# Kernel tuning notes

Hardware: AMD Instinct MI355X
Metric: run time of the kernel (lower is better)

## Reference

```python
import jax, jax.numpy as jnp
import numpy as np
import math

B, T, H, W, C = 2, 8, 32, 32, 512
DEPTH = 2
HEADS = 16
GH = 8            # global FAVOR+ heads (first GH heads, as in performer-pytorch)
DH = C // HEADS   # 32
WIN = C // 8      # 64 = local window size
FF = 2 * C
NB_F = int(DH * math.log(DH))  # 110 random features (performer default)


def _ortho_proj(m, d, rng):
    # gaussian orthogonal random matrix, scaling=0 (row norms ~ chi(d))
    blocks = []
    for _ in range(m // d + 1):
        q, _ = np.linalg.qr(rng.standard_normal((d, d)))
        blocks.append(q.T)
    Q = np.concatenate(blocks, 0)[:m]
    mult = np.linalg.norm(rng.standard_normal((m, d)), axis=1)
    return (mult[:, None] * Q).astype(np.float32)


def setup_inputs():
    rng = np.random.default_rng(0)
    g = lambda *s: jnp.asarray(rng.standard_normal(s) * 0.02, jnp.float32)
    z = lambda *s: jnp.zeros(s, jnp.float32)
    o = lambda *s: jnp.ones(s, jnp.float32)
    p = {}
    p["x"] = jnp.asarray(rng.standard_normal((B, T, H, W, C)), jnp.float32)
    p["ln1_g"], p["ln1_b"] = o(DEPTH, C), z(DEPTH, C)
    p["Wq"], p["bq"] = g(DEPTH, C, C), z(DEPTH, C)
    p["Wk"], p["bk"] = g(DEPTH, C, C), z(DEPTH, C)
    p["Wv"], p["bv"] = g(DEPTH, C, C), z(DEPTH, C)
    p["Wo"], p["bo"] = g(DEPTH, C, C), z(DEPTH, C)
    p["proj"] = jnp.asarray(np.stack([_ortho_proj(NB_F, DH, rng) for _ in range(DEPTH)]))
    p["ln2_g"], p["ln2_b"] = o(DEPTH, C), z(DEPTH, C)
    p["W1"], p["b1"] = g(DEPTH, C, FF), z(DEPTH, FF)
    p["W2"], p["b2"] = g(DEPTH, FF, C), z(DEPTH, C)
    return p


def _ln(x, g, b):
    m = x.mean(-1, keepdims=True)
    v = x.var(-1, keepdims=True)
    return (x - m) / jnp.sqrt(v + 1e-5) * g + b


def _softmax_kernel(x, proj, is_query):
    # FAVOR+ positive softmax features. x: [b,h,n,d], proj: [m,d]
    d = x.shape[-1]
    m = proj.shape[0]
    dn = d ** -0.25
    dd = jnp.einsum('bhnd,md->bhnm', x * dn, proj)
    diag = jnp.sum(x * x, -1, keepdims=True) * 0.5 * (dn * dn)
    if is_query:
        stab = jnp.max(dd, axis=-1, keepdims=True)
    else:
        stab = jnp.max(dd, axis=(-1, -2), keepdims=True)
    return (m ** -0.5) * (jnp.exp(dd - diag - stab) + 1e-4)


def _rot_half(x):
    x1, x2 = jnp.split(x, 2, axis=-1)
    return jnp.concatenate([-x2, x1], axis=-1)


def _local_attn(q, k, v, win=WIN):
    # non-causal sliding window, look_backward=1, look_forward=1
    b, hh, n, d = q.shape
    nw = n // win
    qb = q.reshape(b, hh, nw, win, d)
    kb = k.reshape(b, hh, nw, win, d)
    vb = v.reshape(b, hh, nw, win, d)

    def look(t):
        p = jnp.pad(t, ((0, 0), (0, 0), (1, 1), (0, 0), (0, 0)))
        return jnp.concatenate([p[:, :, :-2], p[:, :, 1:-1], p[:, :, 2:]], 3)

    kk, vv = look(kb), look(vb)
    posb = jnp.arange(n).reshape(nw, win)
    pp = jnp.pad(posb, ((1, 1), (0, 0)), constant_values=-1)
    kpos = jnp.concatenate([pp[:-2], pp[1:-1], pp[2:]], 1)
    mask = (kpos == -1)[None, None, :, None, :]
    s = jnp.einsum('bhwid,bhwjd->bhwij', qb * (d ** -0.5), kk)
    s = jnp.where(mask, -1e9, s)
    a = jax.nn.softmax(s, axis=-1)
    o = jnp.einsum('bhwij,bhwjd->bhwid', a, vv)
    return o.reshape(b, hh, n, d)


def _forward(x, ln1_g, ln1_b, Wq, bq, Wk, bk, Wv, bv, Wo, bo, proj, ln2_g, ln2_b, W1, b1, W2, b2):
    Bx, Tx, Hx, Wx, Cx = x.shape
    n = Tx * Hx * Wx
    h = x.reshape(Bx, n, Cx)
    # rotary rel-pos for local heads (local-attention rel_pos_emb_config)
    inv_freq = 1.0 / (10000.0 ** (jnp.arange(0, DH, 2, dtype=jnp.float32) / DH))
    freqs = jnp.arange(n, dtype=jnp.float32)[:, None] * inv_freq[None, :]
    emb = jnp.concatenate([freqs, freqs], -1)
    sin, cos = jnp.sin(emb), jnp.cos(emb)

    for l in range(DEPTH):
        y = _ln(h, ln1_g[l], ln1_b[l])
        q = (y @ Wq[l] + bq[l]).reshape(Bx, n, HEADS, DH).transpose(0, 2, 1, 3)
        k = (y @ Wk[l] + bk[l]).reshape(Bx, n, HEADS, DH).transpose(0, 2, 1, 3)
        v = (y @ Wv[l] + bv[l]).reshape(Bx, n, HEADS, DH).transpose(0, 2, 1, 3)
        gq, lq = q[:, :GH], q[:, GH:]
        gk, lk = k[:, :GH], k[:, GH:]
        gv, lv = v[:, :GH], v[:, GH:]
        # global: FAVOR+ linear attention
        qp = _softmax_kernel(gq, proj[l], True)
        kp = _softmax_kernel(gk, proj[l], False)
        Dinv = 1.0 / jnp.einsum('bhnm,bhm->bhn', qp, kp.sum(-2))
        ctx = jnp.einsum('bhnm,bhnd->bhmd', kp, gv)
        og = jnp.einsum('bhmd,bhnm,bhn->bhnd', ctx, qp, Dinv)
        # local: windowed attention with rotary pos emb
        lqr = lq * cos + _rot_half(lq) * sin
        lkr = lk * cos + _rot_half(lk) * sin
        ol = _local_attn(lqr, lkr, lv)
        o = jnp.concatenate([og, ol], 1).transpose(0, 2, 1, 3).reshape(Bx, n, Cx)
        h = h + o @ Wo[l] + bo[l]
        y = _ln(h, ln2_g[l], ln2_b[l])
        h = h + jax.nn.gelu(y @ W1[l] + b1[l], approximate=False) @ W2[l] + b2[l]
    return h.reshape(Bx, Tx, Hx, Wx, Cx)


def reference(x, ln1_g, ln1_b, Wq, bq, Wk, bk, Wv, bv, Wo, bo, proj, ln2_g, ln2_b, W1, b1, W2, b2):
    return _forward(x, ln1_g, ln1_b, Wq, bq, Wk, bk, Wv, bv, Wo, bo, proj, ln2_g, ln2_b, W1, b1, W2, b2)
```

## Files before the change

kernel.cpp:

```cpp
#include <hip/hip_runtime.h>
#include <math.h>

namespace {

constexpr int BATCH = 2;
constexpr int NTOK  = 8192;
constexpr int MROWS = 16384;
constexpr int C     = 512;
constexpr int GH    = 8;
constexpr int DH    = 32;
constexpr int WIN   = 64;
constexpr int NW    = 128;
constexpr int FF    = 1024;
constexpr int NBF   = 110;
constexpr int NBFP  = 128;

constexpr float F_DN     = 0.42044820762685725f;
constexpr float F_RNORM  = 0.09534625892455924f;
constexpr float F_LSCALE = 0.17677669529663687f;

typedef __attribute__((ext_vector_type(8))) short bf16x8;
typedef __attribute__((ext_vector_type(4))) float f32x4;

__device__ __forceinline__ ushort f2b(float f){
  unsigned u = __float_as_uint(f);
  unsigned r = u + 0x7FFFu + ((u >> 16) & 1u);
  return (ushort)(r >> 16);
}
__device__ __forceinline__ float b2f(ushort u){
  return __uint_as_float((unsigned)u << 16);
}

__device__ __forceinline__ void gload16(const void* g, void* l){
  __builtin_amdgcn_global_load_lds((const __attribute__((address_space(1))) void*)g,
                                   (__attribute__((address_space(3))) void*)l, 16, 0, 0);
}

__global__ void k_tables(float* __restrict__ cost, float* __restrict__ sint){
  int idx = blockIdx.x*256 + threadIdx.x;
  if (idx >= NTOK*16) return;
  int pos = idx >> 4, f = idx & 15;
  float inv = powf(10000.f, -(float)f/16.f);
  float ang = (float)pos * inv;
  cost[idx] = cosf(ang);
  sint[idx] = sinf(ang);
}

__global__ __launch_bounds__(256) void k_wcvt_all(const float* __restrict__ Wq, const float* __restrict__ Wk,
     const float* __restrict__ Wv, const float* __restrict__ Wo, const float* __restrict__ W1,
     const float* __restrict__ W2, ushort* __restrict__ wt){
  __shared__ float t[32][33];
  int id = blockIdx.x;
  int l = id >> 11;
  int r = id & 2047;
  const float* src; ushort* dst; int K, N, bx, by;
  if (r < 1024){
    int mat = r >> 8, tt = r & 255;
    bx = tt & 15; by = tt >> 4; K = 512; N = 512;
    src = ((mat == 0) ? Wq : (mat == 1) ? Wk : (mat == 2) ? Wv : Wo) + (size_t)l*262144;
    dst = wt + (size_t)l*2097152 + (size_t)mat*262144;
  } else if (r < 1536){
    int tt = r - 1024;
    bx = tt & 31; by = tt >> 5; K = 512; N = 1024;
    src = W1 + (size_t)l*524288;
    dst = wt + (size_t)l*2097152 + 1048576;
  } else {
    int tt = r - 1536;
    bx = tt & 15; by = tt >> 4; K = 1024; N = 512;
    src = W2 + (size_t)l*524288;
    dst = wt + (size_t)l*2097152 + 1572864;
  }
  int tx = threadIdx.x & 31, ty = threadIdx.x >> 5;
  #pragma unroll
  for (int rr = ty; rr < 32; rr += 8) t[rr][tx] = src[(size_t)(by*32+rr)*N + bx*32 + tx];
  __syncthreads();
  #pragma unroll
  for (int rr = ty; rr < 32; rr += 8) dst[(size_t)(bx*32+rr)*K + by*32 + tx] = f2b(t[tx][rr]);
}

__global__ __launch_bounds__(256) void k_ln(const float* __restrict__ x, const float* __restrict__ g,
                     const float* __restrict__ b, ushort* __restrict__ y){
  int row = blockIdx.x, t = threadIdx.x;
  const float* xr = x + (size_t)row*C;
  float2 v = *(const float2*)(xr + 2*t);
  float s = v.x + v.y, ss = v.x*v.x + v.y*v.y;
  #pragma unroll
  for (int o = 32; o; o >>= 1){ s += __shfl_down(s, o); ss += __shfl_down(ss, o); }
  __shared__ float rs[4], rss[4];
  int wv = t >> 6, ln = t & 63;
  if (ln == 0){ rs[wv] = s; rss[wv] = ss; }
  __syncthreads();
  float S = rs[0]+rs[1]+rs[2]+rs[3], SS = rss[0]+rss[1]+rss[2]+rss[3];
  float mean = S * (1.f/C);
  float var  = SS * (1.f/C) - mean*mean;
  float rstd = rsqrtf(var + 1e-5f);
  float2 gg = *(const float2*)(g + 2*t);
  float2 bb = *(const float2*)(b + 2*t);
  ushort2 ov;
  ov.x = f2b((v.x - mean)*rstd*gg.x + bb.x);
  ov.y = f2b((v.y - mean)*rstd*gg.y + bb.y);
  *(ushort2*)(y + (size_t)row*C + 2*t) = ov;
}

template<int ACT, int OBF, int QKV>
__global__ __launch_bounds__(256) void k_mgemm(const ushort* __restrict__ A, const ushort* __restrict__ Bt,
      const float* __restrict__ bias, const float* __restrict__ bias2, const float* __restrict__ bias3,
      const float* __restrict__ res, float* __restrict__ outf, ushort* __restrict__ outb,
      const float* __restrict__ cosT, const float* __restrict__ sinT, int Nd, int Kd){
  __shared__ ushort As[2][128*32];
  __shared__ ushort Bs[2][128*32];
  int tid = threadIdx.x;
  int lane = tid & 63, wave = tid >> 6;
  int wr = wave >> 1, wc = wave & 1;
  int gx = gridDim.x;
  int nwg = gx * (int)gridDim.y;
  int bid = (int)(blockIdx.y*gx + blockIdx.x);
  int swz = (bid & 7)*(nwg >> 3) + (bid >> 3);
  int row0 = (swz / gx)*128, col0 = (swz % gx)*128;
  f32x4 acc[4][4] = {};
  int nt = Kd >> 5;

  #define STAGE(buf, kt) {                                                        \
    int k0_ = (kt)*32;                                                            \
    _Pragma("unroll")                                                             \
    for (int cc = 0; cc < 2; cc++){                                               \
      int off = (wave*2 + cc)*1024 + lane*16;                                     \
      int r_ = off >> 6, ke_ = (off & 63) >> 1;                                   \
      gload16(A  + (size_t)(row0 + r_)*Kd + k0_ + ke_,                            \
              (char*)As[buf] + (wave*2 + cc)*1024);                               \
      gload16(Bt + (size_t)(col0 + r_)*Kd + k0_ + ke_,                            \
              (char*)Bs[buf] + (wave*2 + cc)*1024);                               \
    }                                                                             \
  }

  STAGE(0, 0);
  __syncthreads();

  for (int t = 0; t < nt; t++){
    int cur = t & 1;
    bf16x8 af[4], bfr[4];
    #pragma unroll
    for (int m = 0; m < 4; m++)
      af[m] = *(const bf16x8*)((const char*)As[cur] + (wr*64 + m*16 + (lane&15))*64 + (lane>>4)*16);
    #pragma unroll
    for (int n = 0; n < 4; n++)
      bfr[n] = *(const bf16x8*)((const char*)Bs[cur] + (wc*64 + n*16 + (lane&15))*64 + (lane>>4)*16);
    if (t + 1 < nt) STAGE(cur^1, t+1);
    __builtin_amdgcn_s_setprio(1);
    #pragma unroll
    for (int m = 0; m < 4; m++)
      #pragma unroll
      for (int n = 0; n < 4; n++)
        acc[m][n] = __builtin_amdgcn_mfma_f32_16x16x32_bf16(af[m], bfr[n], acc[m][n], 0, 0, 0);
    __builtin_amdgcn_s_setprio(0);
    __syncthreads();
  }
  #undef STAGE

  if (QKV){
    #pragma unroll
    for (int m = 0; m < 4; m++){
      int rbase = row0 + wr*64 + m*16 + (lane>>4)*4;
      #pragma unroll
      for (int np = 0; np < 2; np++){
        int n0 = 2*np, n1 = n0 + 1;
        int ccol = col0 + wc*64 + n0*16 + (lane&15);
        int bid2 = ccol >> 9;
        int cl  = ccol & 511;
        const float* bp = (bid2 == 0) ? bias : (bid2 == 1) ? bias2 : bias3;
        float b0 = bp[cl], b1 = bp[cl+16];
        bool dorope = (bid2 < 2) && (cl >= 256);
        ushort* obase = outb + (size_t)bid2*MROWS*C;
        int d = lane & 15;
        #pragma unroll
        for (int r = 0; r < 4; r++){
          int grow = rbase + r;
          float a  = acc[m][n0][r] + b0;
          float bb = acc[m][n1][r] + b1;
          if (dorope){
            int pos = grow & (NTOK-1);
            float cv = cosT[pos*16 + d], sv = sinT[pos*16 + d];
            float na = a*cv - bb*sv;
            float nb = bb*cv + a*sv;
            a = na; bb = nb;
          }
          obase[(size_t)grow*C + cl]      = f2b(a);
          obase[(size_t)grow*C + cl + 16] = f2b(bb);
        }
      }
    }
    return;
  }
  #pragma unroll
  for (int m = 0; m < 4; m++){
    int rbase = row0 + wr*64 + m*16 + (lane>>4)*4;
    #pragma unroll
    for (int n = 0; n < 4; n++){
      int ccol = col0 + wc*64 + n*16 + (lane&15);
      float bv = bias[ccol];
      #pragma unroll
      for (int r = 0; r < 4; r++){
        int grow = rbase + r;
        float vv = acc[m][n][r] + bv;
        if (ACT == 1) vv = 0.5f*vv*(1.f + erff(vv*0.7071067811865476f));
        if (res) vv += res[(size_t)grow*Nd + ccol];
        if (OBF) outb[(size_t)grow*Nd + ccol] = f2b(vv);
        else     outf[(size_t)grow*Nd + ccol] = vv;
      }
    }
  }
}

__global__ __launch_bounds__(256) void k_ctx3(const ushort* __restrict__ k, const ushort* __restrict__ v,
        const float* __restrict__ proj, float* __restrict__ ctxp, float* __restrict__ ksump){
  int bh = blockIdx.x >> 5, chunk = blockIdx.x & 31;
  int b = bh >> 3, h = bh & 7;
  __shared__ __align__(16) ushort pl[NBFP*40];
  __shared__ __align__(16) ushort Ps[NBFP*72];
  __shared__ __align__(16) ushort Vt[48*72];
  __shared__ float dgl[256];
  int tid = threadIdx.x;
  int lane = tid & 63, wave = tid >> 6;
  int c = lane & 15, g = lane >> 4;
  int i0 = chunk*256;

  for (int idx = tid; idx < NBFP*32; idx += 256){
    int f = idx >> 5, d = idx & 31;
    pl[f*40 + d] = (f < NBF) ? f2b(proj[f*32 + d]*F_DN) : (ushort)0;
  }
  const ushort* kbase = k + ((size_t)b*NTOK + i0)*C + h*DH;
  const ushort* vbase = v + ((size_t)b*NTOK + i0)*C + h*DH;
  #pragma unroll
  for (int s = 0; s < 4; s++){
    bf16x8 kf = *(const bf16x8*)(kbase + (size_t)(s*64 + wave*16 + c)*C + g*8);
    const ushort* kp_ = (const ushort*)&kf;
    float sq = 0.f;
    #pragma unroll
    for (int j = 0; j < 8; j++){ float vv = b2f(kp_[j]); sq += vv*vv; }
    sq += __shfl_xor(sq, 16);
    sq += __shfl_xor(sq, 32);
    if (g == 0) dgl[s*64 + wave*16 + c] = 0.5f*F_DN*F_DN*sq;
  }
  for (int idx = tid; idx < 15*72; idx += 256) Vt[33*72 + idx] = 0;

  f32x4 zz = {0.f, 0.f, 0.f, 0.f};
  f32x4 acc[2][3] = {};

  for (int s = 0; s < 4; s++){
    __syncthreads();
    {
      int r = tid >> 2, part = tid & 3;
      uint4 vv = *(const uint4*)(vbase + (size_t)(s*64 + r)*C + part*8);
      const ushort* vp = (const ushort*)&vv;
      #pragma unroll
      for (int j = 0; j < 8; j++) Vt[(part*8+j)*72 + r] = vp[j];
      if (tid < 64) Vt[32*72 + tid] = 0x3F80;
    }
    bf16x8 af = *(const bf16x8*)(kbase + (size_t)(s*64 + wave*16 + c)*C + g*8);
    #pragma unroll
    for (int ft = 0; ft < 8; ft++){
      bf16x8 bf = *(const bf16x8*)(pl + (ft*16 + c)*40 + g*8);
      f32x4 dd = __builtin_amdgcn_mfma_f32_16x16x32_bf16(af, bf, zz, 0, 0, 0);
      int feat = ft*16 + c;
      bool fvalid = feat < NBF;
      ushort pb[4];
      #pragma unroll
      for (int r = 0; r < 4; r++){
        float kp = 0.f;
        if (fvalid){
          float dg_ = dgl[s*64 + wave*16 + g*4 + r];
          kp = F_RNORM*(__expf(dd[r] - dg_) + 1e-4f);
        }
        pb[r] = f2b(kp);
      }
      uint2 pd;
      pd.x = (unsigned)pb[0] | ((unsigned)pb[1] << 16);
      pd.y = (unsigned)pb[2] | ((unsigned)pb[3] << 16);
      *(uint2*)(Ps + (ft*16 + c)*72 + wave*16 + g*4) = pd;
    }
    __syncthreads();
    #pragma unroll
    for (int i = 0; i < 2; i++){
      int ft = wave*2 + i;
      #pragma unroll
      for (int kk = 0; kk < 2; kk++){
        bf16x8 ap = *(const bf16x8*)(Ps + (ft*16 + c)*72 + kk*32 + g*8);
        #pragma unroll
        for (int nt = 0; nt < 3; nt++){
          bf16x8 bv = *(const bf16x8*)(Vt + (nt*16 + c)*72 + kk*32 + g*8);
          acc[i][nt] = __builtin_amdgcn_mfma_f32_16x16x32_bf16(ap, bv, acc[i][nt], 0, 0, 0);
        }
      }
    }
  }
  size_t pbase = (size_t)(bh*32 + chunk)*NBF;
  #pragma unroll
  for (int i = 0; i < 2; i++){
    int ftb = (wave*2 + i)*16;
    #pragma unroll
    for (int r = 0; r < 4; r++){
      int feat = ftb + g*4 + r;
      if (feat < NBF){
        #pragma unroll
        for (int nt = 0; nt < 2; nt++)
          ctxp[(pbase + feat)*DH + nt*16 + c] = acc[i][nt][r];
        if (c == 0) ksump[pbase + feat] = acc[i][2][r];
      }
    }
  }
}

__global__ void k_ctxred(const float* __restrict__ ctxp, const float* __restrict__ ksump,
                         float* __restrict__ ctx, float* __restrict__ ksum){
  int bh = blockIdx.x / NBF, m = blockIdx.x % NBF;
  int t = threadIdx.x;
  if (t < DH){
    float s = 0.f;
    for (int c = 0; c < 32; c++) s += ctxp[((size_t)(bh*32 + c)*NBF + m)*DH + t];
    ctx[((size_t)bh*NBF + m)*DH + t] = s;
  } else if (t == DH){
    float s = 0.f;
    for (int c = 0; c < 32; c++) s += ksump[(size_t)(bh*32 + c)*NBF + m];
    ksum[bh*NBF + m] = s;
  }
}

__global__ __launch_bounds__(256) void k_qattn3(const ushort* __restrict__ q, const float* __restrict__ proj,
        const float* __restrict__ ctx, const float* __restrict__ ksum, ushort* __restrict__ o){
  int bh = blockIdx.x >> 7, chunk = blockIdx.x & 127;
  int b = bh >> 3, h = bh & 7;
  __shared__ __align__(16) ushort pl[NBFP*40];
  __shared__ __align__(16) ushort ql[64*40];
  __shared__ __align__(16) ushort ctl[32*136];
  __shared__ __align__(16) ushort Ps[64*136];
  __shared__ float ksl[NBFP];
  __shared__ float dgl[64];
  __shared__ float dvl[64];
  int tid = threadIdx.x;
  int lane = tid & 63, wave = tid >> 6;
  int c = lane & 15, g = lane >> 4;
  int i0 = chunk*64;

  for (int idx = tid; idx < NBFP*32; idx += 256){
    int f = idx >> 5, d = idx & 31;
    pl[f*40 + d] = (f < NBF) ? f2b(proj[f*32 + d]*F_DN) : (ushort)0;
  }
  {
    int row = tid >> 2, part = tid & 3;
    uint4 qq = *(const uint4*)(q + (size_t)(b*NTOK + i0 + row)*C + h*DH + part*8);
    *(uint4*)(ql + row*40 + part*8) = qq;
    const ushort* qp_ = (const ushort*)&qq;
    float sq = 0.f;
    #pragma unroll
    for (int j = 0; j < 8; j++){ float vv = b2f(qp_[j]); sq += vv*vv; }
    sq += __shfl_xor(sq, 1);
    sq += __shfl_xor(sq, 2);
    if (part == 0) dgl[row] = 0.5f*F_DN*F_DN*sq;
  }
  for (int idx = tid; idx < 32*NBFP; idx += 256){
    int d = idx >> 7, f = idx & 127;
    float vv = (f < NBF) ? ctx[((size_t)bh*NBF + f)*DH + d] : 0.f;
    ctl[d*136 + f] = f2b(vv);
  }
  if (tid < NBFP) ksl[tid] = (tid < NBF) ? ksum[bh*NBF + tid] : 0.f;
  __syncthreads();

  f32x4 zz = {0.f, 0.f, 0.f, 0.f};
  bf16x8 qf = *(const bf16x8*)(ql + (wave*16 + c)*40 + g*8);
  f32x4 st[8];
  #pragma unroll
  for (int mt = 0; mt < 8; mt++){
    bf16x8 af = *(const bf16x8*)(pl + (mt*16 + c)*40 + g*8);
    st[mt] = __builtin_amdgcn_mfma_f32_16x16x32_bf16(af, qf, zz, 0, 0, 0);
  }
  float mx = -1e30f;
  #pragma unroll
  for (int mt = 0; mt < 8; mt++)
    #pragma unroll
    for (int r = 0; r < 4; r++){
      int feat = mt*16 + g*4 + r;
      if (feat < NBF) mx = fmaxf(mx, st[mt][r]);
    }
  mx = fmaxf(mx, __shfl_xor(mx, 16));
  mx = fmaxf(mx, __shfl_xor(mx, 32));
  float diagv = dgl[wave*16 + c];
  float dv = 0.f;
  #pragma unroll
  for (int mt = 0; mt < 8; mt++){
    ushort pb[4];
    #pragma unroll
    for (int r = 0; r < 4; r++){
      int feat = mt*16 + g*4 + r;
      float qp = 0.f;
      if (feat < NBF) qp = F_RNORM*(__expf(st[mt][r] - diagv - mx) + 1e-4f);
      ushort qb = f2b(qp);
      pb[r] = qb;
      dv += b2f(qb)*ksl[feat];
    }
    uint2 pd;
    pd.x = (unsigned)pb[0] | ((unsigned)pb[1] << 16);
    pd.y = (unsigned)pb[2] | ((unsigned)pb[3] << 16);
    *(uint2*)(Ps + (wave*16 + c)*136 + mt*16 + g*4) = pd;
  }
  dv += __shfl_xor(dv, 16);
  dv += __shfl_xor(dv, 32);
  if (g == 0) dvl[wave*16 + c] = 1.f/dv;
  __syncthreads();

  #pragma unroll
  for (int n = 0; n < 2; n++){
    f32x4 acc = zz;
    #pragma unroll
    for (int kk = 0; kk < 4; kk++){
      bf16x8 ap = *(const bf16x8*)(Ps  + (wave*16 + c)*136 + kk*32 + g*8);
      bf16x8 bc = *(const bf16x8*)(ctl + (n*16 + c)*136    + kk*32 + g*8);
      acc = __builtin_amdgcn_mfma_f32_16x16x32_bf16(ap, bc, acc, 0, 0, 0);
    }
    #pragma unroll
    for (int r = 0; r < 4; r++){
      int qrow = wave*16 + g*4 + r;
      float val = acc[r]*dvl[qrow];
      o[(size_t)(b*NTOK + i0 + qrow)*C + h*DH + n*16 + c] = f2b(val);
    }
  }
}

__global__ __launch_bounds__(256) void k_local2(const ushort* __restrict__ q, const ushort* __restrict__ k,
        const ushort* __restrict__ v, ushort* __restrict__ o){
  int blk = blockIdx.x;
  int w = blk & (NW-1);
  int rem = blk >> 7;
  int hl = rem & 7, b = rem >> 3;
  int hd = GH + hl;
  __shared__ __align__(16) ushort Ks[192*32];
  __shared__ __align__(16) ushort Vt[32*200];
  __shared__ __align__(16) ushort Ps[4*16*200];
  int tid = threadIdx.x;
  int lane = tid & 63, wave = tid >> 6;
  int c = lane & 15, g = lane >> 4;

  const ushort* kbase = k + (size_t)b*NTOK*C + hd*DH;
  const ushort* vbase = v + (size_t)b*NTOK*C + hd*DH;
  #pragma unroll
  for (int s = 0; s < 3; s++){
    int ch = tid + s*256;
    int row = ch >> 2, part = ch & 3;
    int kp = min(max((w-1)*WIN + row, 0), NTOK-1);
    gload16(kbase + (size_t)kp*C + part*8, (char*)Ks + (s*256 + wave*64)*16);
  }
  #pragma unroll
  for (int s = 0; s < 3; s++){
    int ch = tid + s*256;
    int row = ch >> 2, part = ch & 3;
    int kp = min(max((w-1)*WIN + row, 0), NTOK-1);
    uint4 vv = *(const uint4*)(vbase + (size_t)kp*C + part*8);
    const ushort* vp = (const ushort*)&vv;
    #pragma unroll
    for (int j = 0; j < 8; j++) Vt[(part*8+j)*200 + row] = vp[j];
  }
  int qrow = w*WIN + wave*16 + c;
  bf16x8 qf = *(const bf16x8*)(q + ((size_t)b*NTOK + qrow)*C + hd*DH + g*8);
  asm volatile("s_waitcnt vmcnt(0)" ::: "memory");
  __syncthreads();

  f32x4 zz = {0.f, 0.f, 0.f, 0.f};
  f32x4 st[12];
  #pragma unroll
  for (int t = 0; t < 12; t++){
    bf16x8 af = *(const bf16x8*)(Ks + (16*t + c)*32 + g*8);
    st[t] = __builtin_amdgcn_mfma_f32_16x16x32_bf16(af, qf, zz, 0, 0, 0);
  }
  int t0 = (w == 0) ? 4 : 0;
  int t1 = (w == NW-1) ? 8 : 12;
  float lsum = 0.f;
  ushort* pw = Ps + wave*3200 + c*200;
  #pragma unroll
  for (int t = 0; t < 12; t++){
    bool valid = (t >= t0) && (t < t1);
    float p0 = valid ? __expf(st[t][0]*F_LSCALE) : 0.f;
    float p1 = valid ? __expf(st[t][1]*F_LSCALE) : 0.f;
    float p2 = valid ? __expf(st[t][2]*F_LSCALE) : 0.f;
    float p3 = valid ? __expf(st[t][3]*F_LSCALE) : 0.f;
    lsum += (p0+p1)+(p2+p3);
    uint2 pd;
    pd.x = (unsigned)f2b(p0) | ((unsigned)f2b(p1) << 16);
    pd.y = (unsigned)f2b(p2) | ((unsigned)f2b(p3) << 16);
    *(uint2*)(pw + 16*t + 4*g) = pd;
  }
  lsum += __shfl_xor(lsum, 16);
  lsum += __shfl_xor(lsum, 32);

  f32x4 oc0 = zz, oc1 = zz;
  #pragma unroll
  for (int kb = 0; kb < 6; kb++){
    bf16x8 pf = *(const bf16x8*)(pw + kb*32 + g*8);
    bf16x8 v0 = *(const bf16x8*)(Vt + c*200 + kb*32 + g*8);
    bf16x8 v1 = *(const bf16x8*)(Vt + (16 + c)*200 + kb*32 + g*8);
    oc0 = __builtin_amdgcn_mfma_f32_16x16x32_bf16(v0, pf, oc0, 0, 0, 0);
    oc1 = __builtin_amdgcn_mfma_f32_16x16x32_bf16(v1, pf, oc1, 0, 0, 0);
  }
  float inv = 1.f/lsum;
  ushort* orow = o + ((size_t)b*NTOK + qrow)*C + hd*DH;
  uint2 w0, w1;
  w0.x = (unsigned)f2b(oc0[0]*inv) | ((unsigned)f2b(oc0[1]*inv) << 16);
  w0.y = (unsigned)f2b(oc0[2]*inv) | ((unsigned)f2b(oc0[3]*inv) << 16);
  w1.x = (unsigned)f2b(oc1[0]*inv) | ((unsigned)f2b(oc1[1]*inv) << 16);
  w1.y = (unsigned)f2b(oc1[2]*inv) | ((unsigned)f2b(oc1[3]*inv) << 16);
  *(uint2*)(orow + 4*g)      = w0;
  *(uint2*)(orow + 16 + 4*g) = w1;
}

}

extern "C" void kernel_launch(void* const* d_in, const int* in_sizes, int n_in,
                              void* d_out, int out_size, void* d_ws, size_t ws_size,
                              hipStream_t stream){
  (void)in_sizes; (void)n_in; (void)out_size; (void)ws_size;
  const float* x     = (const float*)d_in[0];
  const float* ln1_g = (const float*)d_in[1];
  const float* ln1_b = (const float*)d_in[2];
  const float* Wq    = (const float*)d_in[3];
  const float* bq    = (const float*)d_in[4];
  const float* Wk    = (const float*)d_in[5];
  const float* bk    = (const float*)d_in[6];
  const float* Wv    = (const float*)d_in[7];
  const float* bv    = (const float*)d_in[8];
  const float* Wo    = (const float*)d_in[9];
  const float* bo    = (const float*)d_in[10];
  const float* proj  = (const float*)d_in[11];
  const float* ln2_g = (const float*)d_in[12];
  const float* ln2_b = (const float*)d_in[13];
  const float* W1    = (const float*)d_in[14];
  const float* b1    = (const float*)d_in[15];
  const float* W2    = (const float*)d_in[16];
  const float* b2    = (const float*)d_in[17];

  float* h = (float*)d_out;
  const size_t MC = (size_t)MROWS*C;
  char* w = (char*)d_ws;
  auto alloc = [&](size_t bytes)->char*{ char* p = w; w += (bytes + 255) & ~(size_t)255; return p; };

  ushort* y16  = (ushort*)alloc(MC*2);
  ushort* qb16 = (ushort*)alloc(MC*2);
  ushort* kb16 = (ushort*)alloc(MC*2);
  ushort* vb16 = (ushort*)alloc(MC*2);
  ushort* o16  = (ushort*)alloc(MC*2);
  ushort* wt   = (ushort*)alloc((size_t)2*2097152*2);
  float*  cost = (float*) alloc((size_t)NTOK*16*4);
  float*  sint = (float*) alloc((size_t)NTOK*16*4);
  float*  ctxb = (float*) alloc((size_t)16*NBF*DH*4);
  float*  ksum = (float*) alloc((size_t)16*NBF*4);

  ushort* mid16 = qb16;
  float*  ctxp  = (float*)o16;
  float*  ksump = ctxp + (size_t)16*32*NBF*DH;

  k_tables<<<(NTOK*16 + 255)/256, 256, 0, stream>>>(cost, sint);
  k_wcvt_all<<<4096, 256, 0, stream>>>(Wq, Wk, Wv, Wo, W1, W2, wt);

  dim3 blk(256);
  dim3 g512(4, 128);
  dim3 gqkv(12, 128);
  dim3 gff(8, 128);

  for (int l = 0; l < 2; l++){
    const float* pj = proj + (size_t)l*NBF*DH;
    ushort* wl  = wt + (size_t)l*2097152;
    ushort* wtq = wl;
    ushort* wto = wl +  786432;
    ushort* wt1 = wl + 1048576;
    ushort* wt2 = wl + 1572864;
    const float* hin = (l == 0) ? x : h;

    k_ln<<<MROWS, 256, 0, stream>>>(hin, ln1_g + l*C, ln1_b + l*C, y16);
    k_mgemm<0,1,1><<<gqkv, blk, 0, stream>>>(y16, wtq, bq + l*C, bk + l*C, bv + l*C,
                                             nullptr, nullptr, qb16, cost, sint, 1536, C);
    k_ctx3<<<16*32, 256, 0, stream>>>(kb16, vb16, pj, ctxp, ksump);
    k_ctxred<<<16*NBF, 64, 0, stream>>>(ctxp, ksump, ctxb, ksum);
    k_qattn3<<<16*128, 256, 0, stream>>>(qb16, pj, ctxb, ksum, o16);
    k_local2<<<BATCH*8*NW, 256, 0, stream>>>(qb16, kb16, vb16, o16);
    k_mgemm<0,0,0><<<g512, blk, 0, stream>>>(o16, wto, bo + l*C, nullptr, nullptr, hin, h, nullptr,
                                             nullptr, nullptr, C, C);
    k_ln<<<MROWS, 256, 0, stream>>>(h, ln2_g + l*C, ln2_b + l*C, y16);
    k_mgemm<1,1,0><<<gff, blk, 0, stream>>>(y16, wt1, b1 + l*FF, nullptr, nullptr, nullptr,
                                            nullptr, mid16, nullptr, nullptr, FF, C);
    k_mgemm<0,0,0><<<g512, blk, 0, stream>>>(mid16, wt2, b2 + l*C, nullptr, nullptr, h, h, nullptr,
                                             nullptr, nullptr, C, FF);
  }
}
```

Baseline: 507.3 us.

## Enlarge GEMM tiles to 256x128 with 512-thread blocks sharing B tile

The bf16 MFMA GEMM moves from 128x128 tiles with 4 waves to 256x128 tiles with 8 waves. Each wave still computes a 64x64 sub-tile, and the staged B tile is now shared by twice as many rows. Grids are halved in the row dimension and the staging loads are rewritten accordingly. This cuts global traffic for B and block count per FLOP, at the cost of more LDS per block and possibly lower occupancy.

```diff
diff --git a/kernel.cpp b/kernel.cpp
--- a/kernel.cpp
+++ b/kernel.cpp
@@ -103,33 +103,36 @@
 }
 
 template<int ACT, int OBF, int QKV>
-__global__ __launch_bounds__(256) void k_mgemm(const ushort* __restrict__ A, const ushort* __restrict__ Bt,
+__global__ __launch_bounds__(512) void k_mgemm(const ushort* __restrict__ A, const ushort* __restrict__ Bt,
       const float* __restrict__ bias, const float* __restrict__ bias2, const float* __restrict__ bias3,
       const float* __restrict__ res, float* __restrict__ outf, ushort* __restrict__ outb,
       const float* __restrict__ cosT, const float* __restrict__ sinT, int Nd, int Kd){
-  __shared__ ushort As[2][128*32];
+  __shared__ ushort As[2][256*32];
   __shared__ ushort Bs[2][128*32];
   int tid = threadIdx.x;
   int lane = tid & 63, wave = tid >> 6;
+  int c = lane & 15, g = lane >> 4;
   int wr = wave >> 1, wc = wave & 1;
   int gx = gridDim.x;
   int nwg = gx * (int)gridDim.y;
   int bid = (int)(blockIdx.y*gx + blockIdx.x);
   int swz = (bid & 7)*(nwg >> 3) + (bid >> 3);
-  int row0 = (swz / gx)*128, col0 = (swz % gx)*128;
+  int row0 = (swz / gx)*256, col0 = (swz % gx)*128;
   f32x4 acc[4][4] = {};
   int nt = Kd >> 5;
 
   #define STAGE(buf, kt) {                                                        \
     int k0_ = (kt)*32;                                                            \
     _Pragma("unroll")                                                             \
-    for (int cc = 0; cc < 2; cc++){                                               \
-      int off = (wave*2 + cc)*1024 + lane*16;                                     \
-      int r_ = off >> 6, ke_ = (off & 63) >> 1;                                   \
-      gload16(A  + (size_t)(row0 + r_)*Kd + k0_ + ke_,                            \
-              (char*)As[buf] + (wave*2 + cc)*1024);                               \
-      gload16(Bt + (size_t)(col0 + r_)*Kd + k0_ + ke_,                            \
-              (char*)Bs[buf] + (wave*2 + cc)*1024);                               \
+    for (int j = 0; j < 2; j++){                                                  \
+      int ci = j*512 + tid;                                                       \
+      gload16(A + (size_t)(row0 + (ci>>2))*Kd + k0_ + (ci&3)*8,                   \
+              (char*)As[buf] + (j*512 + wave*64)*16);                             \
+    }                                                                             \
+    {                                                                             \
+      int ci = tid;                                                               \
+      gload16(Bt + (size_t)(col0 + (ci>>2))*Kd + k0_ + (ci&3)*8,                  \
+              (char*)Bs[buf] + (wave*64)*16);                                     \
     }                                                                             \
   }
 
@@ -141,10 +144,10 @@
     bf16x8 af[4], bfr[4];
     #pragma unroll
     for (int m = 0; m < 4; m++)
-      af[m] = *(const bf16x8*)((const char*)As[cur] + (wr*64 + m*16 + (lane&15))*64 + (lane>>4)*16);
+      af[m] = *(const bf16x8*)(As[cur] + (wr*64 + m*16 + c)*32 + g*8);
     #pragma unroll
     for (int n = 0; n < 4; n++)
-      bfr[n] = *(const bf16x8*)((const char*)Bs[cur] + (wc*64 + n*16 + (lane&15))*64 + (lane>>4)*16);
+      bfr[n] = *(const bf16x8*)(Bs[cur] + (wc*64 + n*16 + c)*32 + g*8);
     if (t + 1 < nt) STAGE(cur^1, t+1);
     __builtin_amdgcn_s_setprio(1);
     #pragma unroll
@@ -160,18 +163,17 @@
   if (QKV){
     #pragma unroll
     for (int m = 0; m < 4; m++){
-      int rbase = row0 + wr*64 + m*16 + (lane>>4)*4;
+      int rbase = row0 + wr*64 + m*16 + g*4;
       #pragma unroll
       for (int np = 0; np < 2; np++){
         int n0 = 2*np, n1 = n0 + 1;
-        int ccol = col0 + wc*64 + n0*16 + (lane&15);
+        int ccol = col0 + wc*64 + n0*16 + c;
         int bid2 = ccol >> 9;
         int cl  = ccol & 511;
         const float* bp = (bid2 == 0) ? bias : (bid2 == 1) ? bias2 : bias3;
         float b0 = bp[cl], b1 = bp[cl+16];
         bool dorope = (bid2 < 2) && (cl >= 256);
         ushort* obase = outb + (size_t)bid2*MROWS*C;
-        int d = lane & 15;
         #pragma unroll
         for (int r = 0; r < 4; r++){
           int grow = rbase + r;
@@ -179,7 +181,7 @@
           float bb = acc[m][n1][r] + b1;
           if (dorope){
             int pos = grow & (NTOK-1);
-            float cv = cosT[pos*16 + d], sv = sinT[pos*16 + d];
+            float cv = cosT[pos*16 + c], sv = sinT[pos*16 + c];
             float na = a*cv - bb*sv;
             float nb = bb*cv + a*sv;
             a = na; bb = nb;
@@ -193,10 +195,10 @@
   }
   #pragma unroll
   for (int m = 0; m < 4; m++){
-    int rbase = row0 + wr*64 + m*16 + (lane>>4)*4;
+    int rbase = row0 + wr*64 + m*16 + g*4;
     #pragma unroll
     for (int n = 0; n < 4; n++){
-      int ccol = col0 + wc*64 + n*16 + (lane&15);
+      int ccol = col0 + wc*64 + n*16 + c;
       float bv = bias[ccol];
       #pragma unroll
       for (int r = 0; r < 4; r++){
@@ -558,10 +560,10 @@
   k_tables<<<(NTOK*16 + 255)/256, 256, 0, stream>>>(cost, sint);
   k_wcvt_all<<<4096, 256, 0, stream>>>(Wq, Wk, Wv, Wo, W1, W2, wt);
 
-  dim3 blk(256);
-  dim3 g512(4, 128);
-  dim3 gqkv(12, 128);
-  dim3 gff(8, 128);
+  dim3 blkg(512);
+  dim3 g512(4, 64);
+  dim3 gqkv(12, 64);
+  dim3 gff(8, 64);
 
   for (int l = 0; l < 2; l++){
     const float* pj = proj + (size_t)l*NBF*DH;
@@ -573,18 +575,18 @@
     const float* hin = (l == 0) ? x : h;
 
     k_ln<<<MROWS, 256, 0, stream>>>(hin, ln1_g + l*C, ln1_b + l*C, y16);
-    k_mgemm<0,1,1><<<gqkv, blk, 0, stream>>>(y16, wtq, bq + l*C, bk + l*C, bv + l*C,
-                                             nullptr, nullptr, qb16, cost, sint, 1536, C);
+    k_mgemm<0,1,1><<<gqkv, blkg, 0, stream>>>(y16, wtq, bq + l*C, bk + l*C, bv + l*C,
+                                              nullptr, nullptr, qb16, cost, sint, 1536, C);
     k_ctx3<<<16*32, 256, 0, stream>>>(kb16, vb16, pj, ctxp, ksump);
     k_ctxred<<<16*NBF, 64, 0, stream>>>(ctxp, ksump, ctxb, ksum);
     k_qattn3<<<16*128, 256, 0, stream>>>(qb16, pj, ctxb, ksum, o16);
     k_local2<<<BATCH*8*NW, 256, 0, stream>>>(qb16, kb16, vb16, o16);
-    k_mgemm<0,0,0><<<g512, blk, 0, stream>>>(o16, wto, bo + l*C, nullptr, nullptr, hin, h, nullptr,
-                                             nullptr, nullptr, C, C);
+    k_mgemm<0,0,0><<<g512, blkg, 0, stream>>>(o16, wto, bo + l*C, nullptr, nullptr, hin, h, nullptr,
+                                              nullptr, nullptr, C, C);
     k_ln<<<MROWS, 256, 0, stream>>>(h, ln2_g + l*C, ln2_b + l*C, y16);
-    k_mgemm<1,1,0><<<gff, blk, 0, stream>>>(y16, wt1, b1 + l*FF, nullptr, nullptr, nullptr,
-                                            nullptr, mid16, nullptr, nullptr, FF, C);
-    k_mgemm<0,0,0><<<g512, blk, 0, stream>>>(mid16, wt2, b2 + l*C, nullptr, nullptr, h, h, nullptr,
-                                             nullptr, nullptr, C, FF);
-  }
-}
+    k_mgemm<1,1,0><<<gff, blkg, 0, stream>>>(y16, wt1, b1 + l*FF, nullptr, nullptr, nullptr,
+                                             nullptr, mid16, nullptr, nullptr, FF, C);
+    k_mgemm<0,0,0><<<g512, blkg, 0, stream>>>(mid16, wt2, b2 + l*C, nullptr, nullptr, h, h, nullptr,
+                                              nullptr, nullptr, C, FF);
+  }
+}
```

Result: faster. 489.8 us (-3.4%).
